# Performance work log

Measured on AMD Instinct MI355X. Metric: run time of the kernel, lower is better.

## Reference

```python
import jax, jax.numpy as jnp
import numpy as np

B, N, E, H = 2, 2048, 1024, 16
D = E // H


def setup_inputs() -> dict:
    key = jax.random.key(0)
    ks = jax.random.split(key, 10)
    s = 0.02  # small init so softmax is well-conditioned
    return {
        "x": jax.random.normal(ks[0], (B, N, E), jnp.float32),
        "y": jax.random.normal(ks[1], (B, N, E), jnp.float32),
        # W stored as [in, out]; torch Linear computes x @ W_t.T + b, equivalent here.
        "Wq": jax.random.normal(ks[2], (E, E), jnp.float32) * s,
        "bq": jax.random.normal(ks[3], (E,), jnp.float32) * s,
        "Wk": jax.random.normal(ks[4], (E, E), jnp.float32) * s,
        "bk": jax.random.normal(ks[5], (E,), jnp.float32) * s,
        "Wv": jax.random.normal(ks[6], (E, E), jnp.float32) * s,
        "bv": jax.random.normal(ks[7], (E,), jnp.float32) * s,
        "Wo": jax.random.normal(ks[8], (E, E), jnp.float32) * s,
        "bo": jax.random.normal(ks[9], (E,), jnp.float32) * s,
    }


def _split_heads(t):
    # [b, n, (h d)] -> [b, h, n, d]
    b, n, e = t.shape
    return t.reshape(b, n, H, D).transpose(0, 2, 1, 3)


def reference(x, y, Wq, bq, Wk, bk, Wv, bv, Wo, bo):
    q = _split_heads(x @ Wq + bq)          # [b,h,n,d]
    k = _split_heads(y @ Wk + bk)
    v = _split_heads(y @ Wv + bv)
    energy = jnp.einsum('bhqd,bhkd->bhqk', q, k)            # [b,h,n,n]
    # Faithful quirk: softmax first, then divide by sqrt(emb_size).
    scaling = jnp.asarray(E, x.dtype) ** 0.5
    att = jax.nn.softmax(energy, axis=-1) / scaling
    out = jnp.einsum('bhqk,bhkd->bhqd', att, v)             # [b,h,n,d]
    out = out.transpose(0, 2, 1, 3).reshape(x.shape[0], x.shape[1], E)
    return out @ Wo + bo
```

## Files before the change

kernel.cpp:

```cpp
#include <hip/hip_runtime.h>
#include <stdint.h>

#define BATCH 2
#define SEQ   2048
#define EMB   1024
#define NH    16
#define HD    64
#define MROWS (BATCH*SEQ)
#define LOG2E 1.4426950408889634f

using bf16x8 = __attribute__((ext_vector_type(8))) short;
using f32x4  = __attribute__((ext_vector_type(4))) float;
using f32x16 = __attribute__((ext_vector_type(16))) float;

__device__ __forceinline__ unsigned short f2bf(float f) {
  __bf16 b = (__bf16)f;
  return __builtin_bit_cast(unsigned short, b);
}

__device__ __forceinline__ unsigned int cvtpk_bf16(float lo, float hi) {
  unsigned int w;
  asm("v_cvt_pk_bf16_f32 %0, %1, %2" : "=v"(w) : "v"(lo), "v"(hi));
  return w;
}

#if __has_builtin(__builtin_amdgcn_exp2f)
__device__ __forceinline__ float fast_exp2(float x) { return __builtin_amdgcn_exp2f(x); }
#else
__device__ __forceinline__ float fast_exp2(float x) {
  float r;
  asm("v_exp_f32 %0, %1\n\ts_nop 1" : "=v"(r) : "v"(x));
  return r;
}
#endif

__device__ __forceinline__ void swap32(unsigned int& a, unsigned int& b, int hi) {
#if __has_builtin(__builtin_amdgcn_permlane32_swap)
  (void)hi;
  typedef unsigned int u32x2_t __attribute__((ext_vector_type(2)));
  u32x2_t r = __builtin_amdgcn_permlane32_swap(a, b, false, false);
  a = r[0]; b = r[1];
#else
  const unsigned int ca = __shfl_xor(a, 32), cb = __shfl_xor(b, 32);
  const unsigned int na = hi ? cb : a;
  const unsigned int nb = hi ? b : ca;
  a = na; b = nb;
#endif
}

__device__ __forceinline__ float xmax32(float x, int hi) {
  unsigned int a = __builtin_bit_cast(unsigned int, x), b = a;
  swap32(a, b, hi);
  return fmaxf(__builtin_bit_cast(float, a), __builtin_bit_cast(float, b));
}

__device__ __forceinline__ float xadd32(float x, int hi) {
  unsigned int a = __builtin_bit_cast(unsigned int, x), b = a;
  swap32(a, b, hi);
  return __builtin_bit_cast(float, a) + __builtin_bit_cast(float, b);
}

__device__ __forceinline__ void async_load16(const void* g, void* l) {
  __builtin_amdgcn_global_load_lds(
      (__attribute__((address_space(1))) void*)g,
      (__attribute__((address_space(3))) void*)l,
      16, 0, 0);
}

__global__ __launch_bounds__(256) void convert_kernel(
    const float* __restrict__ in, unsigned short* __restrict__ out, int n4) {
  int i = blockIdx.x * blockDim.x + threadIdx.x;
  if (i >= n4) return;
  const float4 v = reinterpret_cast<const float4*>(in)[i];
  ushort4 o;
  o.x = f2bf(v.x); o.y = f2bf(v.y); o.z = f2bf(v.z); o.w = f2bf(v.w);
  reinterpret_cast<ushort4*>(out)[i] = o;
}

__global__ __launch_bounds__(256) void transw_kernel(
    const float* __restrict__ Wq, const float* __restrict__ Wk,
    const float* __restrict__ Wv, const float* __restrict__ Wo,
    unsigned short* __restrict__ WtAll) {
  const int z = blockIdx.z;
  const float* W = (z == 0) ? Wq : (z == 1) ? Wk : (z == 2) ? Wv : Wo;
  unsigned short* Wt = WtAll + (size_t)z * EMB * EMB;
  __shared__ unsigned short tile[64][65];
  const int tc = threadIdx.x & 15;
  const int tr = threadIdx.x >> 4;
  const int n0 = blockIdx.x * 64, k0 = blockIdx.y * 64;
#pragma unroll
  for (int rr = 0; rr < 4; ++rr) {
    const int row = rr * 16 + tr;
    float4 v = *reinterpret_cast<const float4*>(W + (size_t)(k0 + row) * EMB + n0 + tc * 4);
    tile[tc * 4 + 0][row] = f2bf(v.x);
    tile[tc * 4 + 1][row] = f2bf(v.y);
    tile[tc * 4 + 2][row] = f2bf(v.z);
    tile[tc * 4 + 3][row] = f2bf(v.w);
  }
  __syncthreads();
#pragma unroll
  for (int rr = 0; rr < 4; ++rr) {
    const int row = rr * 16 + tr;
    ushort4 o;
    o.x = tile[row][tc * 4 + 0];
    o.y = tile[row][tc * 4 + 1];
    o.z = tile[row][tc * 4 + 2];
    o.w = tile[row][tc * 4 + 3];
    *reinterpret_cast<ushort4*>(Wt + (size_t)(n0 + row) * EMB + k0 + tc * 4) = o;
  }
}

#define BN 128
#define BK 32
#define NKS (EMB/BK)

template <int BMt>
__global__ __launch_bounds__(256, 3) void gemm_kernel(
    const unsigned short* __restrict__ xb,
    const unsigned short* __restrict__ yb,
    const unsigned short* __restrict__ attnb,
    const unsigned short* __restrict__ WtAll,
    const float* __restrict__ bq, const float* __restrict__ bk,
    const float* __restrict__ bv, const float* __restrict__ bo,
    unsigned short* __restrict__ Qb, unsigned short* __restrict__ Kb,
    unsigned short* __restrict__ Vt, float* __restrict__ dout,
    int phase) {
  __shared__ __align__(16) unsigned short As[3][BMt * BK];
  __shared__ __align__(16) unsigned short Bs[3][BN * BK];

  const int z = blockIdx.z;
  const unsigned short* A;
  const unsigned short* Bt;
  const float* bias;
  int mode;
  if (phase == 0) {
    A    = (z == 0) ? xb : yb;
    Bt   = WtAll + (size_t)z * EMB * EMB;
    bias = (z == 0) ? bq : (z == 1) ? bk : bv;
    mode = z;
  } else {
    A = attnb; Bt = WtAll + (size_t)3 * EMB * EMB; bias = bo; mode = 3;
  }

  const int tid = threadIdx.x;
  const int lane = tid & 63, wid = tid >> 6;
  constexpr int WC  = (BMt == 128) ? 2 : 4;
  constexpr int WCW = 128 / WC;
  constexpr int JN  = WCW / 16;
  const int wr = (BMt == 128) ? (wid >> 1) : 0;
  const int wc = (BMt == 128) ? (wid & 1) : wid;
  const int l15 = lane & 15, l4 = lane >> 4;
  const int m0 = blockIdx.y * BMt, n0 = blockIdx.x * BN;

  const int crow = tid >> 2;
  const int cslot = tid & 3;

  auto GSTAGE = [&](int b, int kt) {
    if constexpr (BMt == 128) {
#pragma unroll
      for (int it = 0; it < 2; ++it)
        async_load16(A + (size_t)(m0 + it * 64 + crow) * EMB + kt + cslot * 8,
                     (char*)As[b] + it * 4096 + wid * 1024);
    } else {
      async_load16(A + (size_t)(m0 + crow) * EMB + kt + cslot * 8,
                   (char*)As[b] + wid * 1024);
    }
#pragma unroll
    for (int it = 0; it < 2; ++it)
      async_load16(Bt + (size_t)(n0 + it * 64 + crow) * EMB + kt + cslot * 8,
                   (char*)Bs[b] + it * 4096 + wid * 1024);
  };

  GSTAGE(0, 0);
  GSTAGE(1, BK);

  f32x4 acc[4][JN] = {};

  int buf = 0, sb = 2;
  for (int s = 0; s < NKS; ++s) {
    __builtin_amdgcn_sched_barrier(0);
    if (s < NKS - 1) {
      if constexpr (BMt == 128) {
        asm volatile("s_waitcnt vmcnt(4)" ::: "memory");
      } else {
        asm volatile("s_waitcnt vmcnt(3)" ::: "memory");
      }
    } else {
      asm volatile("s_waitcnt vmcnt(0)" ::: "memory");
    }
    __builtin_amdgcn_s_barrier();
    __builtin_amdgcn_sched_barrier(0);

    if (s + 2 < NKS) { GSTAGE(sb, (s + 2) * BK); }

    bf16x8 af[4], bfr[JN];
#pragma unroll
    for (int i = 0; i < 4; ++i)
      af[i] = *reinterpret_cast<const bf16x8*>(
          (const char*)As[buf] + (wr * 64 + i * 16 + l15) * 64 + l4 * 16);
#pragma unroll
    for (int j = 0; j < JN; ++j)
      bfr[j] = *reinterpret_cast<const bf16x8*>(
          (const char*)Bs[buf] + (wc * WCW + j * 16 + l15) * 64 + l4 * 16);
#pragma unroll
    for (int i = 0; i < 4; ++i)
#pragma unroll
      for (int j = 0; j < JN; ++j)
        acc[i][j] = __builtin_amdgcn_mfma_f32_16x16x32_bf16(af[i], bfr[j], acc[i][j], 0, 0, 0);

    buf = (buf == 2) ? 0 : buf + 1;
    sb  = (sb  == 2) ? 0 : sb + 1;
  }

#pragma unroll
  for (int i = 0; i < 4; ++i) {
#pragma unroll
    for (int j = 0; j < JN; ++j) {
      const int col = n0 + wc * WCW + j * 16 + l15;
      const float bsv = bias[col];
#pragma unroll
      for (int r = 0; r < 4; ++r) {
        const int row = m0 + wr * 64 + i * 16 + l4 * 4 + r;
        const float v = acc[i][j][r] + bsv;
        if (mode == 3) {
          dout[(size_t)row * EMB + col] = v;
        } else {
          const int b = row >> 11, n = row & (SEQ - 1);
          const int h = col >> 6, d = col & (HD - 1);
          if (mode == 0)
            Qb[(((size_t)(b * NH + h)) * SEQ + n) * HD + d] = f2bf(v);
          else if (mode == 1)
            Kb[(((size_t)(b * NH + h)) * SEQ + n) * HD + d] = f2bf(v * LOG2E);
          else
            Vt[(((size_t)(b * NH + h)) * HD + d) * SEQ + n] = f2bf(v);
        }
      }
    }
  }
}

#define KVB 64
#define NT  (SEQ/KVB)

__global__ __launch_bounds__(256, 2) void flash_kernel(
    const unsigned short* __restrict__ Qb,
    const unsigned short* __restrict__ Kb,
    const unsigned short* __restrict__ Vt,
    unsigned short* __restrict__ attnb) {
  __shared__ __align__(16) char Ks[3][8192];
  __shared__ __align__(16) char Vs[3][8192];

  const int tid = threadIdx.x;
  const int lane = tid & 63, wid = tid >> 6;
  const int l31 = lane & 31, hi = lane >> 5;

  const int lin = blockIdx.x;
  const int swz = (lin & 7) * 64 + (lin >> 3);
  const int bh = swz >> 4;
  const int qt = swz & 15;
  const int bb = bh >> 4, hh = bh & 15;
  const int q0 = qt * 128 + wid * 32;

  const unsigned short* Qp = Qb + (size_t)bh * SEQ * HD;
  const unsigned short* Kp = Kb + (size_t)bh * SEQ * HD;
  const unsigned short* Vp = Vt + (size_t)bh * HD * SEQ;

  const int srow = tid >> 3;
  const int sslot = tid & 7;

  bf16x8 qf[4];
#pragma unroll
  for (int kt = 0; kt < 4; ++kt)
    qf[kt] = *reinterpret_cast<const bf16x8*>(Qp + (size_t)(q0 + l31) * HD + kt * 16 + hi * 8);

#define STAGE(b, kv)                                                        \
  {                                                                         \
    _Pragma("unroll")                                                       \
    for (int it = 0; it < 2; ++it) {                                        \
      const int r = it * 32 + srow;                                         \
      async_load16(Kp + (size_t)((kv) + r) * HD + ((sslot ^ (r & 7)) * 8),  \
                   Ks[b] + it * 4096 + tid * 16);                           \
      async_load16(Vp + (size_t)r * SEQ + (kv) + ((sslot ^ (r & 7)) * 8),   \
                   Vs[b] + it * 4096 + tid * 16);                           \
    }                                                                       \
  }

  STAGE(0, 0)
  STAGE(1, KVB)

  f32x16 accO[2] = {};
  float mI = -1e30f, lI = 0.f;

  int buf = 0, sb = 2;
  for (int t = 0; t < NT; ++t) {
    __builtin_amdgcn_sched_barrier(0);
    if (t < NT - 1) {
      asm volatile("s_waitcnt vmcnt(4)" ::: "memory");
    } else {
      asm volatile("s_waitcnt vmcnt(0)" ::: "memory");
    }
    __builtin_amdgcn_s_barrier();
    __builtin_amdgcn_sched_barrier(0);

    if (t + 2 < NT) { STAGE(sb, (t + 2) * KVB) }

    bf16x8 kf[2][4];
#pragma unroll
    for (int t2 = 0; t2 < 2; ++t2)
#pragma unroll
      for (int kt = 0; kt < 4; ++kt) {
        const int key = t2 * 32 + l31;
        kf[t2][kt] = *reinterpret_cast<const bf16x8*>(
            Ks[buf] + key * 128 + (((kt * 2 + hi) ^ (key & 7)) * 16));
      }
    f32x16 sc[2] = {};
#pragma unroll
    for (int t2 = 0; t2 < 2; ++t2)
#pragma unroll
      for (int kt = 0; kt < 4; ++kt)
        sc[t2] = __builtin_amdgcn_mfma_f32_32x32x16_bf16(kf[t2][kt], qf[kt], sc[t2], 0, 0, 0);

    float mown = sc[0][0];
#pragma unroll
    for (int t2 = 0; t2 < 2; ++t2)
#pragma unroll
      for (int r = 0; r < 16; ++r) mown = fmaxf(mown, sc[t2][r]);
    mown = xmax32(mown, hi);

    if (!__all(mown - mI <= 8.0f)) {
      const float mnew = fmaxf(mI, mown);
      const float scl = fast_exp2(mI - mnew);
      mI = mnew;
      lI *= scl;
#pragma unroll
      for (int dt = 0; dt < 2; ++dt)
#pragma unroll
        for (int r = 0; r < 16; ++r) accO[dt][r] *= scl;
    }

    float p[2][16];
    float ls = 0.f;
#pragma unroll
    for (int t2 = 0; t2 < 2; ++t2)
#pragma unroll
      for (int r = 0; r < 16; ++r) {
        p[t2][r] = fast_exp2(sc[t2][r] - mI);
        ls += p[t2][r];
      }
    lI += xadd32(ls, hi);

    bf16x8 pf[4];
#pragma unroll
    for (int kt = 0; kt < 4; ++kt) {
      const int t2 = kt >> 1, g = (kt & 1) * 8;
      unsigned int Aw = cvtpk_bf16(p[t2][g + 0], p[t2][g + 1]);
      unsigned int Cw = cvtpk_bf16(p[t2][g + 2], p[t2][g + 3]);
      unsigned int Bw = cvtpk_bf16(p[t2][g + 4], p[t2][g + 5]);
      unsigned int Dw = cvtpk_bf16(p[t2][g + 6], p[t2][g + 7]);
      swap32(Aw, Bw, hi);
      swap32(Cw, Dw, hi);
      union { unsigned int u[4]; bf16x8 v; } cvt;
      cvt.u[0] = Aw; cvt.u[1] = Cw; cvt.u[2] = Bw; cvt.u[3] = Dw;
      pf[kt] = cvt.v;
    }

    bf16x8 vf[2][4];
#pragma unroll
    for (int dt = 0; dt < 2; ++dt)
#pragma unroll
      for (int kt = 0; kt < 4; ++kt) {
        const int d = dt * 32 + l31;
        vf[dt][kt] = *reinterpret_cast<const bf16x8*>(
            Vs[buf] + d * 128 + (((kt * 2 + hi) ^ (d & 7)) * 16));
      }
#pragma unroll
    for (int dt = 0; dt < 2; ++dt)
#pragma unroll
      for (int kt = 0; kt < 4; ++kt)
        accO[dt] = __builtin_amdgcn_mfma_f32_32x32x16_bf16(vf[dt][kt], pf[kt], accO[dt], 0, 0, 0);

    buf = (buf == 2) ? 0 : buf + 1;
    sb  = (sb  == 2) ? 0 : sb + 1;
  }
#undef STAGE

  const float inv = 1.0f / (lI * 32.0f);
  const size_t obase = ((size_t)(bb * SEQ + q0 + l31)) * EMB + hh * HD;
#pragma unroll
  for (int dt = 0; dt < 2; ++dt)
#pragma unroll
    for (int rr = 0; rr < 4; ++rr) {
      ushort4 o;
      o.x = f2bf(accO[dt][rr * 4 + 0] * inv);
      o.y = f2bf(accO[dt][rr * 4 + 1] * inv);
      o.z = f2bf(accO[dt][rr * 4 + 2] * inv);
      o.w = f2bf(accO[dt][rr * 4 + 3] * inv);
      *reinterpret_cast<ushort4*>(attnb + obase + dt * 32 + 8 * rr + 4 * hi) = o;
    }
}

extern "C" void kernel_launch(void* const* d_in, const int* in_sizes, int n_in,
                              void* d_out, int out_size, void* d_ws, size_t ws_size,
                              hipStream_t stream) {
  (void)in_sizes; (void)n_in; (void)out_size;
  const float* x  = (const float*)d_in[0];
  const float* y  = (const float*)d_in[1];
  const float* Wq = (const float*)d_in[2];
  const float* bq = (const float*)d_in[3];
  const float* Wk = (const float*)d_in[4];
  const float* bk = (const float*)d_in[5];
  const float* Wv = (const float*)d_in[6];
  const float* bv = (const float*)d_in[7];
  const float* Wo = (const float*)d_in[8];
  const float* bo = (const float*)d_in[9];
  float* out = (float*)d_out;

  char* ws = (char*)d_ws;
  unsigned short* xb    = (unsigned short*)(ws + (size_t)(0u  << 20));
  unsigned short* yb    = (unsigned short*)(ws + (size_t)(8u  << 20));
  unsigned short* WtAll = (unsigned short*)(ws + (size_t)(16u << 20));
  unsigned short* Qb    = (unsigned short*)(ws + (size_t)(24u << 20));
  unsigned short* Kb    = (unsigned short*)(ws + (size_t)(32u << 20));
  unsigned short* Vt    = (unsigned short*)(ws + (size_t)(40u << 20));
  unsigned short* attnb = (unsigned short*)(ws + (size_t)(48u << 20));
  if (ws_size < ((size_t)56u << 20)) return;

  const int n4 = (BATCH * SEQ * EMB) / 4;
  hipLaunchKernelGGL(convert_kernel, dim3(n4 / 256), dim3(256), 0, stream, x, xb, n4);
  hipLaunchKernelGGL(convert_kernel, dim3(n4 / 256), dim3(256), 0, stream, y, yb, n4);
  hipLaunchKernelGGL(transw_kernel, dim3(16, 16, 4), dim3(256), 0, stream, Wq, Wk, Wv, Wo, WtAll);
  hipLaunchKernelGGL((gemm_kernel<128>), dim3(EMB / BN, MROWS / 128, 3), dim3(256), 0, stream,
                     xb, yb, attnb, WtAll, bq, bk, bv, bo, Qb, Kb, Vt, out, 0);
  hipLaunchKernelGGL(flash_kernel, dim3(SEQ / 128 * BATCH * NH), dim3(256), 0, stream,
                     Qb, Kb, Vt, attnb);
  hipLaunchKernelGGL((gemm_kernel<64>), dim3(EMB / BN, MROWS / 64, 1), dim3(256), 0, stream,
                     xb, yb, attnb, WtAll, bq, bk, bv, bo, Qb, Kb, Vt, out, 1);
}
```

Before: 132.7 us.

## Process two 32-row query tiles per wave in flash attention

Each wave now handles 64 query rows (two 32-row subtiles) instead of 32, so the workgroup covers 256 queries. Every K and V fragment read from LDS is reused across twice as many MFMAs, and half as many workgroups stage the same K/V data. The grid shrinks to 256 blocks and launch bounds drop to one block per SIMD set to make room for the doubled accumulators and score registers, which lowers occupancy and leaves about one block per CU.

Measured after the change: 147.8 us. 11.4% more time.

```diff
diff --git a/kernel.cpp b/kernel.cpp
--- a/kernel.cpp
+++ b/kernel.cpp
@@ -242,7 +242,7 @@
 #define KVB 64
 #define NT  (SEQ/KVB)
 
-__global__ __launch_bounds__(256, 2) void flash_kernel(
+__global__ __launch_bounds__(256, 1) void flash_kernel(
     const unsigned short* __restrict__ Qb,
     const unsigned short* __restrict__ Kb,
     const unsigned short* __restrict__ Vt,
@@ -255,11 +255,11 @@
   const int l31 = lane & 31, hi = lane >> 5;
 
   const int lin = blockIdx.x;
-  const int swz = (lin & 7) * 64 + (lin >> 3);
-  const int bh = swz >> 4;
-  const int qt = swz & 15;
+  const int swz = (lin & 7) * 32 + (lin >> 3);
+  const int bh = swz >> 3;
+  const int qt = swz & 7;
   const int bb = bh >> 4, hh = bh & 15;
-  const int q0 = qt * 128 + wid * 32;
+  const int q0 = qt * 256 + wid * 64;
 
   const unsigned short* Qp = Qb + (size_t)bh * SEQ * HD;
   const unsigned short* Kp = Kb + (size_t)bh * SEQ * HD;
@@ -268,10 +268,13 @@
   const int srow = tid >> 3;
   const int sslot = tid & 7;
 
-  bf16x8 qf[4];
-#pragma unroll
-  for (int kt = 0; kt < 4; ++kt)
-    qf[kt] = *reinterpret_cast<const bf16x8*>(Qp + (size_t)(q0 + l31) * HD + kt * 16 + hi * 8);
+  bf16x8 qf[2][4];
+#pragma unroll
+  for (int qq = 0; qq < 2; ++qq)
+#pragma unroll
+    for (int kt = 0; kt < 4; ++kt)
+      qf[qq][kt] = *reinterpret_cast<const bf16x8*>(
+          Qp + (size_t)(q0 + qq * 32 + l31) * HD + kt * 16 + hi * 8);
 
 #define STAGE(b, kv)                                                        \
   {                                                                         \
@@ -288,8 +291,8 @@
   STAGE(0, 0)
   STAGE(1, KVB)
 
-  f32x16 accO[2] = {};
-  float mI = -1e30f, lI = 0.f;
+  f32x16 accO[2][2] = {};
+  float mI[2] = {-1e30f, -1e30f}, lI[2] = {0.f, 0.f};
 
   int buf = 0, sb = 2;
   for (int t = 0; t < NT; ++t) {
@@ -313,56 +316,70 @@
         kf[t2][kt] = *reinterpret_cast<const bf16x8*>(
             Ks[buf] + key * 128 + (((kt * 2 + hi) ^ (key & 7)) * 16));
       }
-    f32x16 sc[2] = {};
-#pragma unroll
-    for (int t2 = 0; t2 < 2; ++t2)
-#pragma unroll
-      for (int kt = 0; kt < 4; ++kt)
-        sc[t2] = __builtin_amdgcn_mfma_f32_32x32x16_bf16(kf[t2][kt], qf[kt], sc[t2], 0, 0, 0);
-
-    float mown = sc[0][0];
-#pragma unroll
-    for (int t2 = 0; t2 < 2; ++t2)
-#pragma unroll
-      for (int r = 0; r < 16; ++r) mown = fmaxf(mown, sc[t2][r]);
-    mown = xmax32(mown, hi);
-
-    if (!__all(mown - mI <= 8.0f)) {
-      const float mnew = fmaxf(mI, mown);
-      const float scl = fast_exp2(mI - mnew);
-      mI = mnew;
-      lI *= scl;
-#pragma unroll
-      for (int dt = 0; dt < 2; ++dt)
-#pragma unroll
-        for (int r = 0; r < 16; ++r) accO[dt][r] *= scl;
-    }
-
-    float p[2][16];
-    float ls = 0.f;
-#pragma unroll
-    for (int t2 = 0; t2 < 2; ++t2)
-#pragma unroll
-      for (int r = 0; r < 16; ++r) {
-        p[t2][r] = fast_exp2(sc[t2][r] - mI);
-        ls += p[t2][r];
-      }
-    lI += xadd32(ls, hi);
-
-    bf16x8 pf[4];
-#pragma unroll
-    for (int kt = 0; kt < 4; ++kt) {
-      const int t2 = kt >> 1, g = (kt & 1) * 8;
-      unsigned int Aw = cvtpk_bf16(p[t2][g + 0], p[t2][g + 1]);
-      unsigned int Cw = cvtpk_bf16(p[t2][g + 2], p[t2][g + 3]);
-      unsigned int Bw = cvtpk_bf16(p[t2][g + 4], p[t2][g + 5]);
-      unsigned int Dw = cvtpk_bf16(p[t2][g + 6], p[t2][g + 7]);
-      swap32(Aw, Bw, hi);
-      swap32(Cw, Dw, hi);
-      union { unsigned int u[4]; bf16x8 v; } cvt;
-      cvt.u[0] = Aw; cvt.u[1] = Cw; cvt.u[2] = Bw; cvt.u[3] = Dw;
-      pf[kt] = cvt.v;
-    }
+    f32x16 sc[2][2] = {};
+#pragma unroll
+    for (int qq = 0; qq < 2; ++qq)
+#pragma unroll
+      for (int t2 = 0; t2 < 2; ++t2)
+#pragma unroll
+        for (int kt = 0; kt < 4; ++kt)
+          sc[qq][t2] = __builtin_amdgcn_mfma_f32_32x32x16_bf16(kf[t2][kt], qf[qq][kt], sc[qq][t2], 0, 0, 0);
+
+    float mown[2];
+#pragma unroll
+    for (int qq = 0; qq < 2; ++qq) {
+      float m = sc[qq][0][0];
+#pragma unroll
+      for (int t2 = 0; t2 < 2; ++t2)
+#pragma unroll
+        for (int r = 0; r < 16; ++r) m = fmaxf(m, sc[qq][t2][r]);
+      mown[qq] = xmax32(m, hi);
+    }
+
+    const float grow = fmaxf(mown[0] - mI[0], mown[1] - mI[1]);
+    if (!__all(grow <= 8.0f)) {
+#pragma unroll
+      for (int qq = 0; qq < 2; ++qq) {
+        const float mnew = fmaxf(mI[qq], mown[qq]);
+        const float scl = fast_exp2(mI[qq] - mnew);
+        mI[qq] = mnew;
+        lI[qq] *= scl;
+#pragma unroll
+        for (int dt = 0; dt < 2; ++dt)
+#pragma unroll
+          for (int r = 0; r < 16; ++r) accO[qq][dt][r] *= scl;
+      }
+    }
+
+#pragma unroll
+    for (int qq = 0; qq < 2; ++qq) {
+      float ls = 0.f;
+#pragma unroll
+      for (int t2 = 0; t2 < 2; ++t2)
+#pragma unroll
+        for (int r = 0; r < 16; ++r) {
+          sc[qq][t2][r] = fast_exp2(sc[qq][t2][r] - mI[qq]);
+          ls += sc[qq][t2][r];
+        }
+      lI[qq] += xadd32(ls, hi);
+    }
+
+    bf16x8 pf[2][4];
+#pragma unroll
+    for (int qq = 0; qq < 2; ++qq)
+#pragma unroll
+      for (int kt = 0; kt < 4; ++kt) {
+        const int t2 = kt >> 1, g = (kt & 1) * 8;
+        unsigned int Aw = cvtpk_bf16(sc[qq][t2][g + 0], sc[qq][t2][g + 1]);
+        unsigned int Cw = cvtpk_bf16(sc[qq][t2][g + 2], sc[qq][t2][g + 3]);
+        unsigned int Bw = cvtpk_bf16(sc[qq][t2][g + 4], sc[qq][t2][g + 5]);
+        unsigned int Dw = cvtpk_bf16(sc[qq][t2][g + 6], sc[qq][t2][g + 7]);
+        swap32(Aw, Bw, hi);
+        swap32(Cw, Dw, hi);
+        union { unsigned int u[4]; bf16x8 v; } cvt;
+        cvt.u[0] = Aw; cvt.u[1] = Cw; cvt.u[2] = Bw; cvt.u[3] = Dw;
+        pf[qq][kt] = cvt.v;
+      }
 
     bf16x8 vf[2][4];
 #pragma unroll
@@ -374,29 +391,34 @@
             Vs[buf] + d * 128 + (((kt * 2 + hi) ^ (d & 7)) * 16));
       }
 #pragma unroll
-    for (int dt = 0; dt < 2; ++dt)
-#pragma unroll
-      for (int kt = 0; kt < 4; ++kt)
-        accO[dt] = __builtin_amdgcn_mfma_f32_32x32x16_bf16(vf[dt][kt], pf[kt], accO[dt], 0, 0, 0);
+    for (int qq = 0; qq < 2; ++qq)
+#pragma unroll
+      for (int dt = 0; dt < 2; ++dt)
+#pragma unroll
+        for (int kt = 0; kt < 4; ++kt)
+          accO[qq][dt] = __builtin_amdgcn_mfma_f32_32x32x16_bf16(vf[dt][kt], pf[qq][kt], accO[qq][dt], 0, 0, 0);
 
     buf = (buf == 2) ? 0 : buf + 1;
     sb  = (sb  == 2) ? 0 : sb + 1;
   }
 #undef STAGE
 
-  const float inv = 1.0f / (lI * 32.0f);
-  const size_t obase = ((size_t)(bb * SEQ + q0 + l31)) * EMB + hh * HD;
-#pragma unroll
-  for (int dt = 0; dt < 2; ++dt)
-#pragma unroll
-    for (int rr = 0; rr < 4; ++rr) {
-      ushort4 o;
-      o.x = f2bf(accO[dt][rr * 4 + 0] * inv);
-      o.y = f2bf(accO[dt][rr * 4 + 1] * inv);
-      o.z = f2bf(accO[dt][rr * 4 + 2] * inv);
-      o.w = f2bf(accO[dt][rr * 4 + 3] * inv);
-      *reinterpret_cast<ushort4*>(attnb + obase + dt * 32 + 8 * rr + 4 * hi) = o;
-    }
+#pragma unroll
+  for (int qq = 0; qq < 2; ++qq) {
+    const float inv = 1.0f / (lI[qq] * 32.0f);
+    const size_t obase = ((size_t)(bb * SEQ + q0 + qq * 32 + l31)) * EMB + hh * HD;
+#pragma unroll
+    for (int dt = 0; dt < 2; ++dt)
+#pragma unroll
+      for (int rr = 0; rr < 4; ++rr) {
+        ushort4 o;
+        o.x = f2bf(accO[qq][dt][rr * 4 + 0] * inv);
+        o.y = f2bf(accO[qq][dt][rr * 4 + 1] * inv);
+        o.z = f2bf(accO[qq][dt][rr * 4 + 2] * inv);
+        o.w = f2bf(accO[qq][dt][rr * 4 + 3] * inv);
+        *reinterpret_cast<ushort4*>(attnb + obase + dt * 32 + 8 * rr + 4 * hi) = o;
+      }
+  }
 }
 
 extern "C" void kernel_launch(void* const* d_in, const int* in_sizes, int n_in,
@@ -431,7 +453,7 @@
   hipLaunchKernelGGL(transw_kernel, dim3(16, 16, 4), dim3(256), 0, stream, Wq, Wk, Wv, Wo, WtAll);
   hipLaunchKernelGGL((gemm_kernel<128>), dim3(EMB / BN, MROWS / 128, 3), dim3(256), 0, stream,
                      xb, yb, attnb, WtAll, bq, bk, bv, bo, Qb, Kb, Vt, out, 0);
-  hipLaunchKernelGGL(flash_kernel, dim3(SEQ / 128 * BATCH * NH), dim3(256), 0, stream,
+  hipLaunchKernelGGL(flash_kernel, dim3(SEQ / 256 * BATCH * NH), dim3(256), 0, stream,
                      Qb, Kb, Vt, attnb);
   hipLaunchKernelGGL((gemm_kernel<64>), dim3(EMB / BN, MROWS / 64, 1), dim3(256), 0, stream,
                      xb, yb, attnb, WtAll, bq, bk, bv, bo, Qb, Kb, Vt, out, 1);
```
